# Kernel optimization log

Measured on AMD Instinct MI355X. Metric: run time of the kernel, lower is better.

The kernel has to match this reference:

```python
import jax, jax.numpy as jnp
import numpy as np

# Llama-7B FFN up-proj quantized with HQQ 4-bit, group_size=64, axis=0
OUT, IN, GS = 11008, 4096, 64
G = OUT * IN // GS  # 704512 groups


def setup_inputs() -> dict:
    key = jax.random.key(0)
    k1, k2, k3, k4, k5 = jax.random.split(key, 5)
    # packed 4-bit weights: two nibbles per byte, shape [GS//2, G]
    W_q = jax.random.randint(k1, (GS // 2, G), 0, 256, dtype=jnp.int32)
    # per-group scale (meta['scale'] = 1/scale from quantize) and zero
    scale = jax.random.uniform(k2, (1, G), jnp.float32, minval=1e-3, maxval=1e-2)
    zero = jax.random.uniform(k3, (1, G), jnp.float32, minval=0.0, maxval=15.0)
    # decode-style activations: 8 sequences, 1 token each
    x = jax.random.normal(k4, (8, 1, IN), dtype=jnp.float32)
    bias = jax.random.normal(k5, (OUT,), dtype=jnp.float32) * 0.01
    return {"W_q": W_q, "scale": scale, "zero": zero, "x": x, "bias": bias}


def reference(W_q, scale, zero, x, bias):
    # BitPack.unpack_4bit_u8: high nibble rows stacked on low nibble rows
    hi = (W_q >> 4) & 0xF
    lo = W_q & 0xF
    W_q_p = jnp.concatenate([hi, lo], axis=0).astype(x.dtype)  # [GS, G]
    # Quantizer.dequantize: (W_q_p - zero) * scale, reshape to weight shape
    W_r = ((W_q_p - zero) * scale).reshape(OUT, IN)  # [out, in]
    # torch.nn.functional.linear(x, W_r, bias)
    return jnp.einsum('bsi,oi->bso', x, W_r) + bias
```

## Files before the change

kernel.cpp:

```cpp
#include <hip/hip_runtime.h>


#define OUT_ 11008
#define IN_ 4096
#define G_ 704512
#define OC_ 172
#define KS 4
#define KC (IN_ / KS)
#define NIT (KC / 256)

__global__ __launch_bounds__(256, 3)
void hqq_gemv(const int* __restrict__ Wq, const float* __restrict__ scale,
              const float* __restrict__ zero, const float* __restrict__ x,
              float* __restrict__ ws) {
    __shared__ float s_lds[KC];
    __shared__ float z_lds[KC];
    __shared__ float x_lds[8 * KC];

    const int lane = threadIdx.x;
    const int ty   = threadIdx.y;
    const int tid  = ty * 64 + lane;
    const int oc   = blockIdx.y;
    const int ks   = blockIdx.z;
    const int rq0  = blockIdx.x * 16 + ty * 4;

    const int kbase = ks * KC;
    const long gb = (long)oc * IN_ + kbase;
    const int i0 = lane * 4;

    const int* __restrict__ wq0 = Wq + (long)rq0 * G_ + gb;

    int4 qc[4], qn[4];
#pragma unroll
    for (int r = 0; r < 4; ++r) qc[r] = *(const int4*)(wq0 + (long)r * G_ + i0);
#pragma unroll
    for (int r = 0; r < 4; ++r) qn[r] = *(const int4*)(wq0 + (long)r * G_ + i0 + 256);

    {
        const int off = tid * 4;
        *(float4*)(s_lds + off) = *(const float4*)(scale + gb + off);
        *(float4*)(z_lds + off) = *(const float4*)(zero + gb + off);
    }
#pragma unroll
    for (int r = 0; r < 8; ++r) {
        const int off = r * 1024 + tid * 4;
        const int b = off >> 10;
        const int k = off & (KC - 1);
        *(float4*)(x_lds + off) = *(const float4*)(x + b * IN_ + kbase + k);
    }

    __syncthreads();

    float acc[8][8];
#pragma unroll
    for (int r = 0; r < 8; ++r)
#pragma unroll
        for (int b = 0; b < 8; ++b) acc[r][b] = 0.f;

#pragma unroll
    for (int it = 0; it < NIT; ++it) {
        const int i = it * 256 + i0;

        int4 q[4];
#pragma unroll
        for (int r = 0; r < 4; ++r) q[r] = qc[r];
#pragma unroll
        for (int r = 0; r < 4; ++r) qc[r] = qn[r];
        if (it + 2 < NIT) {
#pragma unroll
            for (int r = 0; r < 4; ++r)
                qn[r] = *(const int4*)(wq0 + (long)r * G_ + i + 512);
        }

        const float4 s4 = *(const float4*)(s_lds + i);
        const float4 z4 = *(const float4*)(z_lds + i);
        const float ss[4] = {s4.x, s4.y, s4.z, s4.w};
        const float zs[4] = {-z4.x * s4.x, -z4.y * s4.y, -z4.z * s4.z, -z4.w * s4.w};

        float w[8][4];
#pragma unroll
        for (int rr = 0; rr < 4; ++rr) {
            const int qs[4] = {q[rr].x, q[rr].y, q[rr].z, q[rr].w};
#pragma unroll
            for (int j = 0; j < 4; ++j) {
                w[rr * 2 + 0][j] = fmaf((float)((qs[j] >> 4) & 0xF), ss[j], zs[j]);
                w[rr * 2 + 1][j] = fmaf((float)( qs[j]       & 0xF), ss[j], zs[j]);
            }
        }
#pragma unroll
        for (int b = 0; b < 8; ++b) {
            const float4 xb = *(const float4*)(x_lds + b * KC + i);
#pragma unroll
            for (int r = 0; r < 8; ++r) {
                float a = acc[r][b];
                a = fmaf(xb.x, w[r][0], a);
                a = fmaf(xb.y, w[r][1], a);
                a = fmaf(xb.z, w[r][2], a);
                a = fmaf(xb.w, w[r][3], a);
                acc[r][b] = a;
            }
        }
    }

#pragma unroll
    for (int r = 0; r < 8; ++r)
#pragma unroll
        for (int b = 0; b < 8; ++b) {
            float v = acc[r][b];
#pragma unroll
            for (int off = 32; off > 0; off >>= 1)
                v += __shfl_down(v, off, 64);
            acc[r][b] = v;
        }

    if (lane == 0) {
        float* __restrict__ wp = ws + (long)ks * 8 * OUT_;
#pragma unroll
        for (int rr = 0; rr < 4; ++rr) {
            const int o_hi = (rq0 + rr) * OC_ + oc;
            const int o_lo = (rq0 + rr + 32) * OC_ + oc;
#pragma unroll
            for (int b = 0; b < 8; ++b) {
                wp[b * OUT_ + o_hi] = acc[rr * 2 + 0][b];
                wp[b * OUT_ + o_lo] = acc[rr * 2 + 1][b];
            }
        }
    }
}

__global__ void hqq_reduce(const float* __restrict__ ws,
                           const float* __restrict__ bias,
                           float* __restrict__ out) {
    const int t = blockIdx.x * 256 + threadIdx.x;
    if (t >= 8 * OUT_) return;
    const int o = t % OUT_;
    float v = bias[o];
#pragma unroll
    for (int k = 0; k < KS; ++k) v += ws[k * 8 * OUT_ + t];
    out[t] = v;
}

extern "C" void kernel_launch(void* const* d_in, const int* in_sizes, int n_in,
                              void* d_out, int out_size, void* d_ws, size_t ws_size,
                              hipStream_t stream) {
    const int*   Wq    = (const int*)d_in[0];
    const float* scale = (const float*)d_in[1];
    const float* zero  = (const float*)d_in[2];
    const float* x     = (const float*)d_in[3];
    const float* bias  = (const float*)d_in[4];
    float* out = (float*)d_out;
    float* ws  = (float*)d_ws;

    dim3 grid(2, OC_, KS);
    dim3 block(64, 4);
    hqq_gemv<<<grid, block, 0, stream>>>(Wq, scale, zero, x, ws);
    hqq_reduce<<<(8 * OUT_ + 255) / 256, 256, 0, stream>>>(ws, bias, out);
}
```

Before: 157.9 us.

## Stream packed weights through double-buffered LDS with async global-to-LDS copies

The weight prefetch moves from per-thread register double-buffering to 256-column tiles. These are copied straight into a two-stage LDS buffer with `global_load_lds` (16-byte async copies), and x/scale/zero are staged the same way. The split-K factor goes from 4 to 8, doubling the block count to give more parallelism for this bandwidth-bound GEMV. The inner loop is reordered to load all x vectors once per tile and dequantize one row pair at a time. In exchange, LDS use per block grows, a barrier is added per tile, the reduction workspace doubles, and correctness depends on the async copies completing before the barrier.

After: 171.4 us. 8.6% more time.

```diff
diff --git a/kernel.cpp b/kernel.cpp
--- a/kernel.cpp
+++ b/kernel.cpp
@@ -1,54 +1,58 @@
 #include <hip/hip_runtime.h>
+#include <stdint.h>
 
 
 #define OUT_ 11008
 #define IN_ 4096
 #define G_ 704512
 #define OC_ 172
-#define KS 4
+#define KS 8
 #define KC (IN_ / KS)
-#define NIT (KC / 256)
+#define TILE 256
+#define NT (KC / TILE)
+
+__device__ __forceinline__ void async_cp16(const void* gsrc, void* ldst) {
+    __builtin_amdgcn_global_load_lds(
+        (const __attribute__((address_space(1))) void*)gsrc,
+        (__attribute__((address_space(3))) void*)ldst, 16, 0, 0);
+}
 
 __global__ __launch_bounds__(256, 3)
 void hqq_gemv(const int* __restrict__ Wq, const float* __restrict__ scale,
               const float* __restrict__ zero, const float* __restrict__ x,
               float* __restrict__ ws) {
+    __shared__ float x_lds[8 * KC];
     __shared__ float s_lds[KC];
     __shared__ float z_lds[KC];
-    __shared__ float x_lds[8 * KC];
+    __shared__ int   wq_lds[2][16 * TILE];
 
     const int lane = threadIdx.x;
     const int ty   = threadIdx.y;
-    const int tid  = ty * 64 + lane;
     const int oc   = blockIdx.y;
     const int ks   = blockIdx.z;
-    const int rq0  = blockIdx.x * 16 + ty * 4;
+    const int rqb  = blockIdx.x * 16;
 
     const int kbase = ks * KC;
     const long gb = (long)oc * IN_ + kbase;
-    const int i0 = lane * 4;
 
-    const int* __restrict__ wq0 = Wq + (long)rq0 * G_ + gb;
-
-    int4 qc[4], qn[4];
 #pragma unroll
-    for (int r = 0; r < 4; ++r) qc[r] = *(const int4*)(wq0 + (long)r * G_ + i0);
-#pragma unroll
-    for (int r = 0; r < 4; ++r) qn[r] = *(const int4*)(wq0 + (long)r * G_ + i0 + 256);
-
+    for (int j = 0; j < 4; ++j) {
+        const int fl = j * 1024 + ty * 256;
+        const int b  = fl >> 9;
+        const int k  = fl & (KC - 1);
+        async_cp16(x + b * IN_ + kbase + k + lane * 4, x_lds + fl);
+    }
     {
-        const int off = tid * 4;
-        *(float4*)(s_lds + off) = *(const float4*)(scale + gb + off);
-        *(float4*)(z_lds + off) = *(const float4*)(zero + gb + off);
+        const float* src = (ty < 2 ? scale : zero) + gb + (ty & 1) * 256 + lane * 4;
+        float*       dst = (ty < 2 ? s_lds : z_lds) + (ty & 1) * 256;
+        async_cp16(src, dst);
     }
 #pragma unroll
-    for (int r = 0; r < 8; ++r) {
-        const int off = r * 1024 + tid * 4;
-        const int b = off >> 10;
-        const int k = off & (KC - 1);
-        *(float4*)(x_lds + off) = *(const float4*)(x + b * IN_ + kbase + k);
+    for (int j = 0; j < 4; ++j) {
+        const int row = j * 4 + ty;
+        async_cp16(Wq + (long)(rqb + row) * G_ + gb + lane * 4,
+                   &wq_lds[0][row * TILE]);
     }
-
     __syncthreads();
 
     float acc[8][8];
@@ -57,49 +61,55 @@
 #pragma unroll
         for (int b = 0; b < 8; ++b) acc[r][b] = 0.f;
 
+    const int i0 = lane * 4;
+
+    for (int t = 0; t < NT; ++t) {
+        const int buf = t & 1;
+        if (t + 1 < NT) {
 #pragma unroll
-    for (int it = 0; it < NIT; ++it) {
-        const int i = it * 256 + i0;
-
-        int4 q[4];
-#pragma unroll
-        for (int r = 0; r < 4; ++r) q[r] = qc[r];
-#pragma unroll
-        for (int r = 0; r < 4; ++r) qc[r] = qn[r];
-        if (it + 2 < NIT) {
-#pragma unroll
-            for (int r = 0; r < 4; ++r)
-                qn[r] = *(const int4*)(wq0 + (long)r * G_ + i + 512);
+            for (int j = 0; j < 4; ++j) {
+                const int row = j * 4 + ty;
+                async_cp16(Wq + (long)(rqb + row) * G_ + gb + (t + 1) * TILE + lane * 4,
+                           &wq_lds[buf ^ 1][row * TILE]);
+            }
         }
 
-        const float4 s4 = *(const float4*)(s_lds + i);
-        const float4 z4 = *(const float4*)(z_lds + i);
+        const int toff = t * TILE;
+        const float4 s4 = *(const float4*)(s_lds + toff + i0);
+        const float4 z4 = *(const float4*)(z_lds + toff + i0);
         const float ss[4] = {s4.x, s4.y, s4.z, s4.w};
         const float zs[4] = {-z4.x * s4.x, -z4.y * s4.y, -z4.z * s4.z, -z4.w * s4.w};
 
-        float w[8][4];
+        float4 xv[8];
+#pragma unroll
+        for (int b = 0; b < 8; ++b)
+            xv[b] = *(const float4*)(x_lds + b * KC + toff + i0);
+
 #pragma unroll
         for (int rr = 0; rr < 4; ++rr) {
-            const int qs[4] = {q[rr].x, q[rr].y, q[rr].z, q[rr].w};
+            const int4 q4 = *(const int4*)&wq_lds[buf][(ty * 4 + rr) * TILE + i0];
+            const int qs[4] = {q4.x, q4.y, q4.z, q4.w};
+            float wh[4], wl[4];
 #pragma unroll
             for (int j = 0; j < 4; ++j) {
-                w[rr * 2 + 0][j] = fmaf((float)((qs[j] >> 4) & 0xF), ss[j], zs[j]);
-                w[rr * 2 + 1][j] = fmaf((float)( qs[j]       & 0xF), ss[j], zs[j]);
+                wh[j] = fmaf((float)((qs[j] >> 4) & 0xF), ss[j], zs[j]);
+                wl[j] = fmaf((float)( qs[j]       & 0xF), ss[j], zs[j]);
+            }
+#pragma unroll
+            for (int b = 0; b < 8; ++b) {
+                const float4 xb = xv[b];
+                float ah = acc[rr * 2 + 0][b];
+                float al = acc[rr * 2 + 1][b];
+                ah = fmaf(xb.x, wh[0], ah); al = fmaf(xb.x, wl[0], al);
+                ah = fmaf(xb.y, wh[1], ah); al = fmaf(xb.y, wl[1], al);
+                ah = fmaf(xb.z, wh[2], ah); al = fmaf(xb.z, wl[2], al);
+                ah = fmaf(xb.w, wh[3], ah); al = fmaf(xb.w, wl[3], al);
+                acc[rr * 2 + 0][b] = ah;
+                acc[rr * 2 + 1][b] = al;
             }
         }
-#pragma unroll
-        for (int b = 0; b < 8; ++b) {
-            const float4 xb = *(const float4*)(x_lds + b * KC + i);
-#pragma unroll
-            for (int r = 0; r < 8; ++r) {
-                float a = acc[r][b];
-                a = fmaf(xb.x, w[r][0], a);
-                a = fmaf(xb.y, w[r][1], a);
-                a = fmaf(xb.z, w[r][2], a);
-                a = fmaf(xb.w, w[r][3], a);
-                acc[r][b] = a;
-            }
-        }
+
+        if (t + 1 < NT) __syncthreads();
     }
 
 #pragma unroll
@@ -117,8 +127,9 @@
         float* __restrict__ wp = ws + (long)ks * 8 * OUT_;
 #pragma unroll
         for (int rr = 0; rr < 4; ++rr) {
-            const int o_hi = (rq0 + rr) * OC_ + oc;
-            const int o_lo = (rq0 + rr + 32) * OC_ + oc;
+            const int rq = rqb + ty * 4 + rr;
+            const int o_hi = rq * OC_ + oc;
+            const int o_lo = (rq + 32) * OC_ + oc;
 #pragma unroll
             for (int b = 0; b < 8; ++b) {
                 wp[b * OUT_ + o_hi] = acc[rr * 2 + 0][b];
```
